# Optimization experiments

Measured on AMD Instinct MI355X. Metric: run time of the kernel, lower is better.

Reference implementation:

```python
import jax, jax.numpy as jnp
import numpy as np

N_NODES = 100000
N_EDGES = 3200000
F_IN, F_HID, F_OUT = 1433, 16, 7


def setup_inputs() -> dict:
    key = jax.random.key(0)
    k1, k2, k3, k4, k5, k6 = jax.random.split(key, 6)
    x = jax.random.normal(k1, (N_NODES, F_IN), dtype=jnp.float32)
    edge_index = jax.random.randint(k2, (2, N_EDGES), 0, N_NODES, dtype=jnp.int64)
    # Glorot-style init for GCNConv weights, zeros for bias (PyG default)
    W1 = jax.random.normal(k3, (F_IN, F_HID), dtype=jnp.float32) * (1.0 / np.sqrt(F_IN))
    b1 = jnp.zeros((F_HID,), dtype=jnp.float32)
    W2 = jax.random.normal(k4, (F_HID, F_OUT), dtype=jnp.float32) * (1.0 / np.sqrt(F_HID))
    b2 = jnp.zeros((F_OUT,), dtype=jnp.float32)
    return {"x": x, "edge_index": edge_index, "W1": W1, "b1": b1, "W2": W2, "b2": b2}


def _gcn_conv(x, W, b, src, dst, deg_inv_sqrt):
    # x: [N, Fin] -> [N, Fout]; src/dst: [E+N] (self-loops included)
    h = x @ W  # linear transform first (PyG GCNConv)
    norm = deg_inv_sqrt[src] * deg_inv_sqrt[dst]  # symmetric normalization
    msg = h[src] * norm[:, None]  # gather + scale
    agg = jax.ops.segment_sum(msg, dst, num_segments=x.shape[0])  # scatter-add at targets
    return agg + b


def reference(x, edge_index, W1, b1, W2, b2):
    n = x.shape[0]
    loops = jnp.arange(n, dtype=edge_index.dtype)
    src = jnp.concatenate([edge_index[0], loops])  # source nodes j
    dst = jnp.concatenate([edge_index[1], loops])  # target nodes i
    # degree over targets (with self-loops), unit edge weights
    deg = jax.ops.segment_sum(jnp.ones_like(src, dtype=x.dtype), dst, num_segments=n)
    deg_inv_sqrt = jnp.where(deg > 0, jax.lax.rsqrt(deg), 0.0)

    h = _gcn_conv(x, W1, b1, src, dst, deg_inv_sqrt)
    h = jax.nn.relu(h)
    # dropout is identity in eval mode
    h = _gcn_conv(h, W2, b2, src, dst, deg_inv_sqrt)
    return jax.nn.log_softmax(h, axis=1)
```

## Files before the change

### kernel.cpp

```cpp
#include <hip/hip_runtime.h>
#include <hip/hip_bf16.h>
#include <hip/hip_cooperative_groups.h>

namespace cg = cooperative_groups;

#define F_IN 1433
#define F_HID 16
#define F_OUT 7
#define KSTEPS 45

typedef __bf16 bf16x8 __attribute__((ext_vector_type(8)));
typedef float f32x4 __attribute__((ext_vector_type(4)));
typedef int i32x4 __attribute__((ext_vector_type(4)));
typedef unsigned short u16;
typedef unsigned int u32;

static __device__ __forceinline__ float bf2f(u16 b) {
    return __builtin_bit_cast(float, (u32)b << 16);
}
static __device__ __forceinline__ u16 f2bf(float f) {
    u32 u = __builtin_bit_cast(u32, f);
    u32 r = u + 0x7FFFu + ((u >> 16) & 1u);
    return (u16)(r >> 16);
}
static __device__ __forceinline__ int clampN(int v, int N) {
    return ((unsigned)v < (unsigned)N) ? v : 0;
}

static __device__ __forceinline__ void subset_bar(int* cnt, int target) {
    __syncthreads();
    if (threadIdx.x == 0) {
        __threadfence();
        __hip_atomic_fetch_add(cnt, 1, __ATOMIC_RELEASE, __HIP_MEMORY_SCOPE_AGENT);
        while (__hip_atomic_load(cnt, __ATOMIC_ACQUIRE, __HIP_MEMORY_SCOPE_AGENT) < target) {
            __builtin_amdgcn_s_sleep(8);
        }
        __threadfence();
    }
    __syncthreads();
}


static __device__ __forceinline__ void dev_stage_lw(const void* W1, int isbf, u16* lw, int tid) {
    const u16* W1u = (const u16*)W1;
    const float* W1f = (const float*)W1;
    for (int idx = tid; idx < KSTEPS * 512; idx += 256) {
        int j = idx & 7, lane = (idx >> 3) & 63, ks = idx >> 9;
        int quad = lane >> 4, n = lane & 15;
        int k = ks * 32 + quad * 8 + j;
        u16 w = 0;
        if (k < F_IN) w = isbf ? W1u[k * 16 + n] : f2bf(W1f[k * 16 + n]);
        lw[idx] = w;
    }
}

template <int ISBF>
static __device__ void dev_gemm(const u16* xu, const float* xf, const u16* lw,
                                float* __restrict__ hn, int N, int tid, int bid, int grid) {
    int wave = tid >> 6, lane = tid & 63;
    int quad = lane >> 4, m = lane & 15;
    int ntiles = (N + 63) / 64;
    int k0 = quad * 8;

    for (int tb = bid; tb < ntiles; tb += grid) {
        int base = tb * 64 + wave * 16;
        int row = base + m;
        int rowc = row < N ? row : N - 1;
        const u16* xru = xu + (size_t)rowc * F_IN;
        const float* xrf = xf + (size_t)rowc * F_IN;

        f32x4 acc = {0.f, 0.f, 0.f, 0.f};
        for (int ks = 0; ks < KSTEPS - 1; ks++) {
            u16 e[8];
            if (ISBF) {
                const u16* xp = xru + k0 + ks * 32;
#pragma unroll
                for (int j = 0; j < 8; j++) e[j] = xp[j];
            } else {
                const float* xp = xrf + k0 + ks * 32;
#pragma unroll
                for (int j = 0; j < 8; j++) e[j] = f2bf(xp[j]);
            }
            i32x4 wv = {(int)((u32)e[0] | ((u32)e[1] << 16)),
                        (int)((u32)e[2] | ((u32)e[3] << 16)),
                        (int)((u32)e[4] | ((u32)e[5] << 16)),
                        (int)((u32)e[6] | ((u32)e[7] << 16))};
            bf16x8 a = __builtin_bit_cast(bf16x8, wv);
            bf16x8 b = __builtin_bit_cast(bf16x8, *(const i32x4*)(&lw[ks * 512 + lane * 8]));
            acc = __builtin_amdgcn_mfma_f32_16x16x32_bf16(a, b, acc, 0, 0, 0);
        }
        {
            int ks = KSTEPS - 1;
            int kb = ks * 32 + k0;
            u16 e[8];
#pragma unroll
            for (int j = 0; j < 8; j++) {
                int k = kb + j;
                e[j] = (k < F_IN) ? (ISBF ? xru[k] : f2bf(xrf[k])) : (u16)0;
            }
            i32x4 wv = {(int)((u32)e[0] | ((u32)e[1] << 16)),
                        (int)((u32)e[2] | ((u32)e[3] << 16)),
                        (int)((u32)e[4] | ((u32)e[5] << 16)),
                        (int)((u32)e[6] | ((u32)e[7] << 16))};
            bf16x8 a = __builtin_bit_cast(bf16x8, wv);
            bf16x8 b = __builtin_bit_cast(bf16x8, *(const i32x4*)(&lw[ks * 512 + lane * 8]));
            acc = __builtin_amdgcn_mfma_f32_16x16x32_bf16(a, b, acc, 0, 0, 0);
        }
#pragma unroll
        for (int r = 0; r < 4; r++) {
            int orow = base + quad * 4 + r;
            if (orow < N) hn[(size_t)orow * 16 + m] = acc[r];
        }
    }
}

static __device__ void dev_agg1(const float* __restrict__ hn, const int* __restrict__ csr,
                                const int* __restrict__ rowoff, const int* __restrict__ deg,
                                const float* __restrict__ dis, const void* __restrict__ b1,
                                const void* __restrict__ W2, int isbf,
                                float* __restrict__ tn, int N, int bid, int grid, int tid) {
    int lane = tid & 63;
    int c = tid & 15, g = tid >> 4;
    float bc = isbf ? bf2f(((const u16*)b1)[c]) : ((const float*)b1)[c];
    float w2c[16];
#pragma unroll
    for (int k = 0; k < 16; k++) {
        float w = 0.f;
        if (c < 7) w = isbf ? bf2f(((const u16*)W2)[k * 7 + c]) : ((const float*)W2)[k * 7 + c];
        w2c[k] = w;
    }
    for (int v = bid * 16 + g; v < N; v += grid * 16) {
        float dv = dis[v];
        float acc = hn[(size_t)v * 16 + c] * dv;
        int s0 = rowoff[v], d = deg[v];
        const int* cp = csr + s0;
        float a1 = 0.f, a2 = 0.f, a3 = 0.f;
        int i = 0;
        for (; i + 4 <= d; i += 4) {
            int sA = clampN(cp[i], N), sB = clampN(cp[i + 1], N);
            int sC = clampN(cp[i + 2], N), sD = clampN(cp[i + 3], N);
            acc += hn[(size_t)sA * 16 + c] * dis[sA];
            a1 += hn[(size_t)sB * 16 + c] * dis[sB];
            a2 += hn[(size_t)sC * 16 + c] * dis[sC];
            a3 += hn[(size_t)sD * 16 + c] * dis[sD];
        }
        for (; i < d; i++) {
            int s = clampN(cp[i], N);
            acc += hn[(size_t)s * 16 + c] * dis[s];
        }
        acc += (a1 + a2) + a3;
        float y = fmaxf(acc * dv + bc, 0.f);
        float s = 0.f;
#pragma unroll
        for (int k = 0; k < 16; k++) s += __shfl(y, (lane & 48) + k, 64) * w2c[k];
        if (c < 8) tn[(size_t)v * 8 + c] = (c < 7) ? s * dv : 0.f;
    }
}

static __device__ void dev_agg2(const float* __restrict__ tn, const int* __restrict__ csr,
                                const int* __restrict__ rowoff, const int* __restrict__ deg,
                                const float* __restrict__ dis, const void* __restrict__ b2,
                                int isbf, void* __restrict__ out, int N, int bid, int grid,
                                int tid) {
    int c = tid & 7, g = tid >> 3;
    float bc = 0.f;
    if (c < 7) bc = isbf ? bf2f(((const u16*)b2)[c]) : ((const float*)b2)[c];
    for (int v = bid * 32 + g; v < N; v += grid * 32) {
        float acc = tn[(size_t)v * 8 + c];
        int s0 = rowoff[v], d = deg[v];
        const int* cp = csr + s0;
        float a1 = 0.f, a2 = 0.f, a3 = 0.f;
        int i = 0;
        for (; i + 4 <= d; i += 4) {
            int sA = clampN(cp[i], N), sB = clampN(cp[i + 1], N);
            int sC = clampN(cp[i + 2], N), sD = clampN(cp[i + 3], N);
            acc += tn[(size_t)sA * 8 + c];
            a1 += tn[(size_t)sB * 8 + c];
            a2 += tn[(size_t)sC * 8 + c];
            a3 += tn[(size_t)sD * 8 + c];
        }
        for (; i < d; i++) acc += tn[(size_t)clampN(cp[i], N) * 8 + c];
        acc += (a1 + a2) + a3;

        float z = (c < 7) ? (acc * dis[v] + bc) : -1e30f;
        float mx = z;
#pragma unroll
        for (int o = 1; o < 8; o <<= 1) mx = fmaxf(mx, __shfl_xor(mx, o, 8));
        float ex = (c < 7) ? expf(z - mx) : 0.f;
        float sm = ex;
#pragma unroll
        for (int o = 1; o < 8; o <<= 1) sm += __shfl_xor(sm, o, 8);
        sm = fmaxf(sm, 1e-30f);
        if (c < 7) {
            float res = z - mx - logf(sm);
            if (isbf)
                ((u16*)out)[(size_t)v * 7 + c] = f2bf(res);
            else
                ((float*)out)[(size_t)v * 7 + c] = res;
        }
    }
}


struct MegaArgs {
    const void* x;
    const int* ei;
    const void* W1;
    const void* b1;
    const void* W2;
    const void* b2;
    int* flags;
    int* cnt;
    int* deg;
    int* rowoff;
    int* fill;
    int* bsum;
    float* dis;
    int* csr;
    float* hn;
    float* tn;
    void* out;
    int N;
    int E;
};

__global__ __launch_bounds__(256) void k_mega(MegaArgs a) {
    cg::grid_group gg = cg::this_grid();
    int tid = threadIdx.x;
    int b = blockIdx.x;
    int G = gridDim.x;

    __shared__ int sflags[2];
    __shared__ __align__(16) u16 lw[KSTEPS * 512];
    __shared__ int sscan[256];
    __shared__ int swsum[4];

    for (int i = b * 256 + tid; i < a.N; i += G * 256) a.deg[i] = 0;
    if (b == 0) {
        if (tid == 0) a.cnt[0] = 0;
        if (tid < 64) {
            u16 v = ((const u16*)a.x)[tid];
            int e = (v >> 7) & 0xFF;
            unsigned long long mb = __ballot(e >= 100 && e <= 140);
            unsigned long long mz = __ballot(a.ei[2 * tid + 1] == 0);
            if (tid == 0) {
                a.flags[0] = (__popcll(mb) >= 56) ? 1 : 0;
                a.flags[1] = (__popcll(mz) >= 48) ? 1 : 0;
            }
        }
    }
    gg.sync();

    if (tid == 0) {
        sflags[0] = a.flags[0];
        sflags[1] = a.flags[1];
    }
    __syncthreads();
    int isbf = sflags[0], sh = sflags[1];

    int G2 = G >> 1;
    int nb = G - G2;
    if (b < G2) {
        dev_stage_lw(a.W1, isbf, lw, tid);
        __syncthreads();
        if (isbf)
            dev_gemm<1>((const u16*)a.x, (const float*)a.x, lw, a.hn, a.N, tid, b, G2);
        else
            dev_gemm<0>((const u16*)a.x, (const float*)a.x, lw, a.hn, a.N, tid, b, G2);
    } else {
        int lb = b - G2;
        for (int i = lb * 256 + tid; i < a.E; i += nb * 256) {
            int d = a.ei[(size_t)(a.E + i) << sh];
            atomicAdd(&a.deg[clampN(d, a.N)], 1);
        }
        subset_bar(a.cnt, nb * 1);
        int chunk = (a.N + nb - 1) / nb;
        int q = (chunk + 255) / 256;
        int base = lb * chunk;
        int nend = base + chunk;
        if (nend > a.N) nend = a.N;
        int tot = 0;
        for (int jj = 0; jj < q; jj++) {
            int node = base + tid * q + jj;
            if (node < nend) tot += a.deg[node];
        }
        sscan[tid] = tot;
        __syncthreads();
        for (int o = 1; o < 256; o <<= 1) {
            int xv = (tid >= o) ? sscan[tid - o] : 0;
            __syncthreads();
            sscan[tid] += xv;
            __syncthreads();
        }
        int incl = sscan[tid];
        if (tid == 255) a.bsum[lb] = incl;
        __syncthreads();
        sscan[tid] = incl - tot;
        subset_bar(a.cnt, nb * 2);
        int part = 0;
        for (int j = tid; j < lb; j += 256) part += a.bsum[j];
        for (int o = 32; o > 0; o >>= 1) part += __shfl_down(part, o, 64);
        if ((tid & 63) == 0) swsum[tid >> 6] = part;
        __syncthreads();
        int off = swsum[0] + swsum[1] + swsum[2] + swsum[3];
        int run = off + sscan[tid];
        for (int jj = 0; jj < q; jj++) {
            int node = base + tid * q + jj;
            if (node < nend) {
                int dn = a.deg[node];
                a.rowoff[node] = run;
                a.fill[node] = run;
                a.dis[node] = rsqrtf((float)(dn + 1));
                run += dn;
            }
        }
        subset_bar(a.cnt, nb * 3);
        for (int i = lb * 256 + tid; i < a.E; i += nb * 256) {
            int d = a.ei[(size_t)(a.E + i) << sh];
            int s = a.ei[(size_t)i << sh];
            int slot = atomicAdd(&a.fill[clampN(d, a.N)], 1);
            if (slot >= 0 && slot < a.E) a.csr[slot] = clampN(s, a.N);
        }
    }
    gg.sync();

    dev_agg1(a.hn, a.csr, a.rowoff, a.deg, a.dis, a.b1, a.W2, isbf, a.tn, a.N, b, G, tid);
    gg.sync();

    dev_agg2(a.tn, a.csr, a.rowoff, a.deg, a.dis, a.b2, isbf, a.out, a.N, b, G, tid);
}


__global__ __launch_bounds__(256) void k_init(const u16* __restrict__ xu,
                                              const int* __restrict__ ei,
                                              int* __restrict__ flags,
                                              int* __restrict__ deg, int N) {
    int i = blockIdx.x * 256 + threadIdx.x;
    if (i < N) deg[i] = 0;
    if (blockIdx.x == 0 && threadIdx.x < 64) {
        int t = threadIdx.x;
        u16 v = xu[t];
        int e = (v >> 7) & 0xFF;
        unsigned long long mb = __ballot(e >= 100 && e <= 140);
        unsigned long long mz = __ballot(ei[2 * t + 1] == 0);
        if (t == 0) {
            flags[0] = (__popcll(mb) >= 56) ? 1 : 0;
            flags[1] = (__popcll(mz) >= 48) ? 1 : 0;
        }
    }
}

__global__ __launch_bounds__(256) void k_deg(const int* __restrict__ ei,
                                             const int* __restrict__ flags,
                                             int* __restrict__ deg, int E, int N) {
    int sh = flags[1];
    int i = blockIdx.x * 256 + threadIdx.x;
    if (i < E) {
        int d = ei[(size_t)(E + i) << sh];
        atomicAdd(&deg[clampN(d, N)], 1);
    }
}

__global__ __launch_bounds__(256) void k_scan1(const int* __restrict__ deg,
                                               int* __restrict__ rowoff,
                                               int* __restrict__ bsum, int N) {
    __shared__ int s[256];
    int t = threadIdx.x, i = blockIdx.x * 256 + t;
    int v = (i < N) ? deg[i] : 0;
    s[t] = v;
    __syncthreads();
    for (int o = 1; o < 256; o <<= 1) {
        int x = 0;
        if (t >= o) x = s[t - o];
        __syncthreads();
        s[t] += x;
        __syncthreads();
    }
    if (i < N) rowoff[i] = s[t] - v;
    if (t == 255) bsum[blockIdx.x] = s[255];
}

__global__ __launch_bounds__(1024) void k_scan2(const int* __restrict__ bsum,
                                                int* __restrict__ bscan, int NB) {
    __shared__ int s[1024];
    int t = threadIdx.x;
    int v = (t < NB) ? bsum[t] : 0;
    s[t] = v;
    __syncthreads();
    for (int o = 1; o < 1024; o <<= 1) {
        int x = 0;
        if (t >= o) x = s[t - o];
        __syncthreads();
        s[t] += x;
        __syncthreads();
    }
    if (t < NB) bscan[t] = s[t] - v;
}

__global__ __launch_bounds__(256) void k_scan3(const int* __restrict__ deg,
                                               int* __restrict__ rowoff,
                                               const int* __restrict__ bscan,
                                               int* __restrict__ fill,
                                               float* __restrict__ dis, int N) {
    int i = blockIdx.x * 256 + threadIdx.x;
    if (i >= N) return;
    int ro = rowoff[i] + bscan[blockIdx.x];
    rowoff[i] = ro;
    fill[i] = ro;
    dis[i] = rsqrtf((float)(deg[i] + 1));
}

__global__ __launch_bounds__(256) void k_fill(const int* __restrict__ ei,
                                              const int* __restrict__ flags,
                                              int* __restrict__ fill,
                                              int* __restrict__ csr, int E, int N) {
    int sh = flags[1];
    int i = blockIdx.x * 256 + threadIdx.x;
    if (i < E) {
        int d = ei[(size_t)(E + i) << sh];
        int s = ei[(size_t)i << sh];
        int slot = atomicAdd(&fill[clampN(d, N)], 1);
        if (slot >= 0 && slot < E) csr[slot] = clampN(s, N);
    }
}

__global__ __launch_bounds__(256) void k_gemm1(const void* __restrict__ x,
                                               const void* __restrict__ W1,
                                               const int* __restrict__ flags,
                                               float* __restrict__ hn, int N) {
    __shared__ __align__(16) u16 lw[KSTEPS * 512];
    int tid = threadIdx.x;
    int isbf = flags[0];
    dev_stage_lw(W1, isbf, lw, tid);
    __syncthreads();
    if (isbf)
        dev_gemm<1>((const u16*)x, (const float*)x, lw, hn, N, tid, blockIdx.x, gridDim.x);
    else
        dev_gemm<0>((const u16*)x, (const float*)x, lw, hn, N, tid, blockIdx.x, gridDim.x);
}

__global__ __launch_bounds__(256) void k_agg1(const float* __restrict__ hn,
                                              const int* __restrict__ csr,
                                              const int* __restrict__ rowoff,
                                              const int* __restrict__ deg,
                                              const float* __restrict__ dis,
                                              const void* __restrict__ b1,
                                              const void* __restrict__ W2,
                                              const int* __restrict__ flags,
                                              float* __restrict__ tn, int N) {
    dev_agg1(hn, csr, rowoff, deg, dis, b1, W2, flags[0], tn, N, blockIdx.x, gridDim.x,
             threadIdx.x);
}

__global__ __launch_bounds__(256) void k_agg2(const float* __restrict__ tn,
                                              const int* __restrict__ csr,
                                              const int* __restrict__ rowoff,
                                              const int* __restrict__ deg,
                                              const float* __restrict__ dis,
                                              const void* __restrict__ b2,
                                              const int* __restrict__ flags,
                                              void* __restrict__ out, int N) {
    dev_agg2(tn, csr, rowoff, deg, dis, b2, flags[0], out, N, blockIdx.x, gridDim.x,
             threadIdx.x);
}


extern "C" void kernel_launch(void* const* d_in, const int* in_sizes, int n_in,
                              void* d_out, int out_size, void* d_ws, size_t ws_size,
                              hipStream_t stream) {
    const void* x = d_in[0];
    const int* ei = (const int*)d_in[1];
    const void* W1 = d_in[2];
    const void* b1 = d_in[3];
    const void* W2 = d_in[4];
    const void* b2 = d_in[5];

    int N = in_sizes[0] / F_IN;
    int E = in_sizes[1] / 2;

    char* p = (char*)d_ws;
    size_t off = 0;
    auto alloc = [&](size_t bytes) -> void* {
        off = (off + 255) & ~(size_t)255;
        void* r = p + off;
        off += bytes;
        return r;
    };
    int* flags = (int*)alloc(256);
    int* cnt = (int*)alloc(256);
    int* deg = (int*)alloc((size_t)N * 4);
    int* rowoff = (int*)alloc((size_t)N * 4);
    int* fill = (int*)alloc((size_t)N * 4);
    int* bsum = (int*)alloc(1024 * 4);
    int* bscan = (int*)alloc(1024 * 4);
    float* dis = (float*)alloc((size_t)N * 4);
    int* csr = (int*)alloc((size_t)E * 4);
    float* hn = (float*)alloc((size_t)N * 16 * 4);
    float* tn = (float*)alloc((size_t)N * 8 * 4);
    (void)ws_size;
    (void)n_in;
    (void)out_size;

    static int s_mb = -1;
    if (s_mb < 0) {
        int mb = 0;
        if (hipOccupancyMaxActiveBlocksPerMultiprocessor(
                &mb, reinterpret_cast<const void*>(&k_mega), 256, 0) != hipSuccess ||
            mb < 1)
            mb = 0;
        s_mb = mb;
    }
    int grid = s_mb * 256;
    if (grid > 1024) grid = 1024;

    bool ok = false;
    if (grid >= 8) {
        MegaArgs ha = {x,    ei,  W1,   b1,  W2, b2,  flags, cnt, deg,
                       rowoff, fill, bsum, dis, csr, hn, tn,  d_out, N,   E};
        void* params[] = {&ha};
        ok = (hipLaunchCooperativeKernel(reinterpret_cast<void*>(&k_mega), dim3(grid),
                                         dim3(256), params, 0, stream) == hipSuccess);
        if (!ok) (void)hipGetLastError();
    }

    if (!ok) {
        int gE = (E + 255) / 256;
        int gN = (N + 255) / 256;
        k_init<<<gN, 256, 0, stream>>>((const u16*)x, ei, flags, deg, N);
        k_deg<<<gE, 256, 0, stream>>>(ei, flags, deg, E, N);
        k_scan1<<<gN, 256, 0, stream>>>(deg, rowoff, bsum, N);
        k_scan2<<<1, 1024, 0, stream>>>(bsum, bscan, gN);
        k_scan3<<<gN, 256, 0, stream>>>(deg, rowoff, bscan, fill, dis, N);
        k_fill<<<gE, 256, 0, stream>>>(ei, flags, fill, csr, E, N);
        int ntiles = (N + 63) / 64;
        int gg = ntiles < 768 ? ntiles : 768;
        k_gemm1<<<gg, 256, 0, stream>>>(x, W1, flags, hn, N);
        k_agg1<<<(N + 15) / 16, 256, 0, stream>>>(hn, csr, rowoff, deg, dis, b1, W2, flags, tn, N);
        k_agg2<<<(N + 31) / 32, 256, 0, stream>>>(tn, csr, rowoff, deg, dis, b2, flags, d_out, N);
    }
}
```

Measured before the change: 1.329 ms.

## Serialize mega-kernel phases with atomic barriers and prescale GEMM output by degree

Replaces the cooperative-launch mega kernel, which overlapped the GEMM on half the grid with CSR construction on the other half, with a normally launched kernel. All blocks now run every phase in sequence, separated by custom atomic grid barriers, and flag detection moves into a tiny pre-kernel. The GEMM now multiplies its output rows by deg^-1/2, so the layer-1 aggregation no longer gathers dis per neighbor, and the A-fragment loads are vectorized and software-prefetched one step ahead. The grid size is now derived from the device's CU count. This relies on all blocks being co-resident without a cooperative launch, and the barriers bail out after a spin limit. It also gives up the GEMM/CSR overlap in exchange for using the full grid in each phase.

Result: slower. 1.732 ms (+30.3%).

```diff
diff --git a/kernel.cpp b/kernel.cpp
--- a/kernel.cpp
+++ b/kernel.cpp
@@ -1,8 +1,5 @@
 #include <hip/hip_runtime.h>
 #include <hip/hip_bf16.h>
-#include <hip/hip_cooperative_groups.h>
-
-namespace cg = cooperative_groups;
 
 #define F_IN 1433
 #define F_HID 16
@@ -27,13 +24,15 @@
     return ((unsigned)v < (unsigned)N) ? v : 0;
 }
 
-static __device__ __forceinline__ void subset_bar(int* cnt, int target) {
+static __device__ __forceinline__ void gbar(int* cnt, int target) {
     __syncthreads();
     if (threadIdx.x == 0) {
         __threadfence();
         __hip_atomic_fetch_add(cnt, 1, __ATOMIC_RELEASE, __HIP_MEMORY_SCOPE_AGENT);
+        unsigned spins = 0;
         while (__hip_atomic_load(cnt, __ATOMIC_ACQUIRE, __HIP_MEMORY_SCOPE_AGENT) < target) {
-            __builtin_amdgcn_s_sleep(8);
+            __builtin_amdgcn_s_sleep(2);
+            if (++spins > (1u << 24)) break;
         }
         __threadfence();
     }
@@ -55,8 +54,29 @@
 }
 
 template <int ISBF>
+static __device__ __forceinline__ i32x4 load_afrag(const u16* xru, const float* xrf, int kb) {
+    if (ISBF) {
+        i32x4 wv;
+        __builtin_memcpy(&wv, xru + kb, 16);
+        return wv;
+    } else {
+        float f[8];
+        __builtin_memcpy(f, xrf + kb, 32);
+        u16 e[8];
+#pragma unroll
+        for (int j = 0; j < 8; j++) e[j] = f2bf(f[j]);
+        i32x4 wv = {(int)((u32)e[0] | ((u32)e[1] << 16)),
+                    (int)((u32)e[2] | ((u32)e[3] << 16)),
+                    (int)((u32)e[4] | ((u32)e[5] << 16)),
+                    (int)((u32)e[6] | ((u32)e[7] << 16))};
+        return wv;
+    }
+}
+
+template <int ISBF>
 static __device__ void dev_gemm(const u16* xu, const float* xf, const u16* lw,
-                                float* __restrict__ hn, int N, int tid, int bid, int grid) {
+                                const float* __restrict__ dis, float* __restrict__ hn,
+                                int N, int tid, int bid, int grid) {
     int wave = tid >> 6, lane = tid & 63;
     int quad = lane >> 4, m = lane & 15;
     int ntiles = (N + 63) / 64;
@@ -70,22 +90,17 @@
         const float* xrf = xf + (size_t)rowc * F_IN;
 
         f32x4 acc = {0.f, 0.f, 0.f, 0.f};
-        for (int ks = 0; ks < KSTEPS - 1; ks++) {
-            u16 e[8];
-            if (ISBF) {
-                const u16* xp = xru + k0 + ks * 32;
-#pragma unroll
-                for (int j = 0; j < 8; j++) e[j] = xp[j];
-            } else {
-                const float* xp = xrf + k0 + ks * 32;
-#pragma unroll
-                for (int j = 0; j < 8; j++) e[j] = f2bf(xp[j]);
-            }
-            i32x4 wv = {(int)((u32)e[0] | ((u32)e[1] << 16)),
-                        (int)((u32)e[2] | ((u32)e[3] << 16)),
-                        (int)((u32)e[4] | ((u32)e[5] << 16)),
-                        (int)((u32)e[6] | ((u32)e[7] << 16))};
-            bf16x8 a = __builtin_bit_cast(bf16x8, wv);
+        i32x4 cur = load_afrag<ISBF>(xru, xrf, k0);
+        for (int ks = 0; ks < KSTEPS - 2; ks++) {
+            i32x4 nxt = load_afrag<ISBF>(xru, xrf, k0 + (ks + 1) * 32);
+            bf16x8 a = __builtin_bit_cast(bf16x8, cur);
+            bf16x8 b = __builtin_bit_cast(bf16x8, *(const i32x4*)(&lw[ks * 512 + lane * 8]));
+            acc = __builtin_amdgcn_mfma_f32_16x16x32_bf16(a, b, acc, 0, 0, 0);
+            cur = nxt;
+        }
+        {
+            int ks = KSTEPS - 2;
+            bf16x8 a = __builtin_bit_cast(bf16x8, cur);
             bf16x8 b = __builtin_bit_cast(bf16x8, *(const i32x4*)(&lw[ks * 512 + lane * 8]));
             acc = __builtin_amdgcn_mfma_f32_16x16x32_bf16(a, b, acc, 0, 0, 0);
         }
@@ -109,7 +124,7 @@
 #pragma unroll
         for (int r = 0; r < 4; r++) {
             int orow = base + quad * 4 + r;
-            if (orow < N) hn[(size_t)orow * 16 + m] = acc[r];
+            if (orow < N) hn[(size_t)orow * 16 + m] = acc[r] * dis[orow];
         }
     }
 }
@@ -130,8 +145,7 @@
         w2c[k] = w;
     }
     for (int v = bid * 16 + g; v < N; v += grid * 16) {
-        float dv = dis[v];
-        float acc = hn[(size_t)v * 16 + c] * dv;
+        float acc = hn[(size_t)v * 16 + c];
         int s0 = rowoff[v], d = deg[v];
         const int* cp = csr + s0;
         float a1 = 0.f, a2 = 0.f, a3 = 0.f;
@@ -139,16 +153,15 @@
         for (; i + 4 <= d; i += 4) {
             int sA = clampN(cp[i], N), sB = clampN(cp[i + 1], N);
             int sC = clampN(cp[i + 2], N), sD = clampN(cp[i + 3], N);
-            acc += hn[(size_t)sA * 16 + c] * dis[sA];
-            a1 += hn[(size_t)sB * 16 + c] * dis[sB];
-            a2 += hn[(size_t)sC * 16 + c] * dis[sC];
-            a3 += hn[(size_t)sD * 16 + c] * dis[sD];
-        }
-        for (; i < d; i++) {
-            int s = clampN(cp[i], N);
-            acc += hn[(size_t)s * 16 + c] * dis[s];
-        }
+            acc += hn[(size_t)sA * 16 + c];
+            a1 += hn[(size_t)sB * 16 + c];
+            a2 += hn[(size_t)sC * 16 + c];
+            a3 += hn[(size_t)sD * 16 + c];
+        }
+        for (; i < d; i++) acc += hn[(size_t)clampN(cp[i], N) * 16 + c];
         acc += (a1 + a2) + a3;
+
+        float dv = dis[v];
         float y = fmaxf(acc * dv + bc, 0.f);
         float s = 0.f;
 #pragma unroll
@@ -202,6 +215,23 @@
 }
 
 
+__global__ __launch_bounds__(64) void k_pre(const u16* __restrict__ xu,
+                                            const int* __restrict__ ei,
+                                            int* __restrict__ flags,
+                                            int* __restrict__ cnt) {
+    int t = threadIdx.x;
+    if (t == 0) cnt[0] = 0;
+    u16 v = xu[t];
+    int e = (v >> 7) & 0xFF;
+    unsigned long long mb = __ballot(e >= 100 && e <= 140);
+    unsigned long long mz = __ballot(ei[2 * t + 1] == 0);
+    if (t == 0) {
+        flags[0] = (__popcll(mb) >= 56) ? 1 : 0;
+        flags[1] = (__popcll(mz) >= 48) ? 1 : 0;
+    }
+}
+
+
 struct MegaArgs {
     const void* x;
     const int* ei;
@@ -224,8 +254,7 @@
     int E;
 };
 
-__global__ __launch_bounds__(256) void k_mega(MegaArgs a) {
-    cg::grid_group gg = cg::this_grid();
+__global__ __launch_bounds__(256) void k_mega2(MegaArgs a) {
     int tid = threadIdx.x;
     int b = blockIdx.x;
     int G = gridDim.x;
@@ -235,22 +264,6 @@
     __shared__ int sscan[256];
     __shared__ int swsum[4];
 
-    for (int i = b * 256 + tid; i < a.N; i += G * 256) a.deg[i] = 0;
-    if (b == 0) {
-        if (tid == 0) a.cnt[0] = 0;
-        if (tid < 64) {
-            u16 v = ((const u16*)a.x)[tid];
-            int e = (v >> 7) & 0xFF;
-            unsigned long long mb = __ballot(e >= 100 && e <= 140);
-            unsigned long long mz = __ballot(a.ei[2 * tid + 1] == 0);
-            if (tid == 0) {
-                a.flags[0] = (__popcll(mb) >= 56) ? 1 : 0;
-                a.flags[1] = (__popcll(mz) >= 48) ? 1 : 0;
-            }
-        }
-    }
-    gg.sync();
-
     if (tid == 0) {
         sflags[0] = a.flags[0];
         sflags[1] = a.flags[1];
@@ -258,27 +271,23 @@
     __syncthreads();
     int isbf = sflags[0], sh = sflags[1];
 
-    int G2 = G >> 1;
-    int nb = G - G2;
-    if (b < G2) {
-        dev_stage_lw(a.W1, isbf, lw, tid);
-        __syncthreads();
-        if (isbf)
-            dev_gemm<1>((const u16*)a.x, (const float*)a.x, lw, a.hn, a.N, tid, b, G2);
-        else
-            dev_gemm<0>((const u16*)a.x, (const float*)a.x, lw, a.hn, a.N, tid, b, G2);
-    } else {
-        int lb = b - G2;
-        for (int i = lb * 256 + tid; i < a.E; i += nb * 256) {
-            int d = a.ei[(size_t)(a.E + i) << sh];
-            atomicAdd(&a.deg[clampN(d, a.N)], 1);
-        }
-        subset_bar(a.cnt, nb * 1);
-        int chunk = (a.N + nb - 1) / nb;
-        int q = (chunk + 255) / 256;
-        int base = lb * chunk;
-        int nend = base + chunk;
-        if (nend > a.N) nend = a.N;
+    dev_stage_lw(a.W1, isbf, lw, tid);
+
+    for (int i = b * 256 + tid; i < a.N; i += G * 256) a.deg[i] = 0;
+    gbar(a.cnt, G * 1);
+
+    for (int i = b * 256 + tid; i < a.E; i += G * 256) {
+        int d = a.ei[(size_t)(a.E + i) << sh];
+        atomicAdd(&a.deg[clampN(d, a.N)], 1);
+    }
+    gbar(a.cnt, G * 2);
+
+    int chunk = (a.N + G - 1) / G;
+    int q = (chunk + 255) / 256;
+    int base = b * chunk;
+    int nend = base + chunk;
+    if (nend > a.N) nend = a.N;
+    {
         int tot = 0;
         for (int jj = 0; jj < q; jj++) {
             int node = base + tid * q + jj;
@@ -293,12 +302,15 @@
             __syncthreads();
         }
         int incl = sscan[tid];
-        if (tid == 255) a.bsum[lb] = incl;
+        if (tid == 255) a.bsum[b] = incl;
         __syncthreads();
         sscan[tid] = incl - tot;
-        subset_bar(a.cnt, nb * 2);
+    }
+    gbar(a.cnt, G * 3);
+
+    {
         int part = 0;
-        for (int j = tid; j < lb; j += 256) part += a.bsum[j];
+        for (int j = tid; j < b; j += 256) part += a.bsum[j];
         for (int o = 32; o > 0; o >>= 1) part += __shfl_down(part, o, 64);
         if ((tid & 63) == 0) swsum[tid >> 6] = part;
         __syncthreads();
@@ -314,18 +326,25 @@
                 run += dn;
             }
         }
-        subset_bar(a.cnt, nb * 3);
-        for (int i = lb * 256 + tid; i < a.E; i += nb * 256) {
-            int d = a.ei[(size_t)(a.E + i) << sh];
-            int s = a.ei[(size_t)i << sh];
-            int slot = atomicAdd(&a.fill[clampN(d, a.N)], 1);
-            if (slot >= 0 && slot < a.E) a.csr[slot] = clampN(s, a.N);
-        }
-    }
-    gg.sync();
+    }
+    gbar(a.cnt, G * 4);
+
+    for (int i = b * 256 + tid; i < a.E; i += G * 256) {
+        int d = a.ei[(size_t)(a.E + i) << sh];
+        int s = a.ei[(size_t)i << sh];
+        int slot = atomicAdd(&a.fill[clampN(d, a.N)], 1);
+        if (slot >= 0 && slot < a.E) a.csr[slot] = clampN(s, a.N);
+    }
+    gbar(a.cnt, G * 5);
+
+    if (isbf)
+        dev_gemm<1>((const u16*)a.x, (const float*)a.x, lw, a.dis, a.hn, a.N, tid, b, G);
+    else
+        dev_gemm<0>((const u16*)a.x, (const float*)a.x, lw, a.dis, a.hn, a.N, tid, b, G);
+    gbar(a.cnt, G * 6);
 
     dev_agg1(a.hn, a.csr, a.rowoff, a.deg, a.dis, a.b1, a.W2, isbf, a.tn, a.N, b, G, tid);
-    gg.sync();
+    gbar(a.cnt, G * 7);
 
     dev_agg2(a.tn, a.csr, a.rowoff, a.deg, a.dis, a.b2, isbf, a.out, a.N, b, G, tid);
 }
@@ -427,6 +446,7 @@
 __global__ __launch_bounds__(256) void k_gemm1(const void* __restrict__ x,
                                                const void* __restrict__ W1,
                                                const int* __restrict__ flags,
+                                               const float* __restrict__ dis,
                                                float* __restrict__ hn, int N) {
     __shared__ __align__(16) u16 lw[KSTEPS * 512];
     int tid = threadIdx.x;
@@ -434,9 +454,9 @@
     dev_stage_lw(W1, isbf, lw, tid);
     __syncthreads();
     if (isbf)
-        dev_gemm<1>((const u16*)x, (const float*)x, lw, hn, N, tid, blockIdx.x, gridDim.x);
+        dev_gemm<1>((const u16*)x, (const float*)x, lw, dis, hn, N, tid, blockIdx.x, gridDim.x);
     else
-        dev_gemm<0>((const u16*)x, (const float*)x, lw, hn, N, tid, blockIdx.x, gridDim.x);
+        dev_gemm<0>((const u16*)x, (const float*)x, lw, dis, hn, N, tid, blockIdx.x, gridDim.x);
 }
 
 __global__ __launch_bounds__(256) void k_agg1(const float* __restrict__ hn,
@@ -491,8 +511,8 @@
     int* deg = (int*)alloc((size_t)N * 4);
     int* rowoff = (int*)alloc((size_t)N * 4);
     int* fill = (int*)alloc((size_t)N * 4);
-    int* bsum = (int*)alloc(1024 * 4);
-    int* bscan = (int*)alloc(1024 * 4);
+    int* bsum = (int*)alloc(2048 * 4);
+    int* bscan = (int*)alloc(2048 * 4);
     float* dis = (float*)alloc((size_t)N * 4);
     int* csr = (int*)alloc((size_t)E * 4);
     float* hn = (float*)alloc((size_t)N * 16 * 4);
@@ -501,29 +521,27 @@
     (void)n_in;
     (void)out_size;
 
-    static int s_mb = -1;
-    if (s_mb < 0) {
-        int mb = 0;
+    static int s_grid = -1;
+    if (s_grid < 0) {
+        int mb = 0, cu = 256;
+        hipDeviceProp_t prop;
+        if (hipGetDeviceProperties(&prop, 0) == hipSuccess && prop.multiProcessorCount > 0)
+            cu = prop.multiProcessorCount;
         if (hipOccupancyMaxActiveBlocksPerMultiprocessor(
-                &mb, reinterpret_cast<const void*>(&k_mega), 256, 0) != hipSuccess ||
+                &mb, reinterpret_cast<const void*>(&k_mega2), 256, 0) != hipSuccess ||
             mb < 1)
             mb = 0;
-        s_mb = mb;
-    }
-    int grid = s_mb * 256;
-    if (grid > 1024) grid = 1024;
-
-    bool ok = false;
-    if (grid >= 8) {
-        MegaArgs ha = {x,    ei,  W1,   b1,  W2, b2,  flags, cnt, deg,
+        int g = mb * cu;
+        if (g > 1024) g = 1024;
+        s_grid = g;
+    }
+
+    if (s_grid >= 16) {
+        MegaArgs ha = {x,    ei,   W1,   b1,  W2,  b2, flags, cnt, deg,
                        rowoff, fill, bsum, dis, csr, hn, tn,  d_out, N,   E};
-        void* params[] = {&ha};
-        ok = (hipLaunchCooperativeKernel(reinterpret_cast<void*>(&k_mega), dim3(grid),
-                                         dim3(256), params, 0, stream) == hipSuccess);
-        if (!ok) (void)hipGetLastError();
-    }
-
-    if (!ok) {
+        k_pre<<<1, 64, 0, stream>>>((const u16*)x, ei, flags, cnt);
+        k_mega2<<<s_grid, 256, 0, stream>>>(ha);
+    } else {
         int gE = (E + 255) / 256;
         int gN = (N + 255) / 256;
         k_init<<<gN, 256, 0, stream>>>((const u16*)x, ei, flags, deg, N);
@@ -534,7 +552,7 @@
         k_fill<<<gE, 256, 0, stream>>>(ei, flags, fill, csr, E, N);
         int ntiles = (N + 63) / 64;
         int gg = ntiles < 768 ? ntiles : 768;
-        k_gemm1<<<gg, 256, 0, stream>>>(x, W1, flags, hn, N);
+        k_gemm1<<<gg, 256, 0, stream>>>(x, W1, flags, dis, hn, N);
         k_agg1<<<(N + 15) / 16, 256, 0, stream>>>(hn, csr, rowoff, deg, dis, b1, W2, flags, tn, N);
         k_agg2<<<(N + 31) / 32, 256, 0, stream>>>(tn, csr, rowoff, deg, dis, b2, flags, d_out, N);
     }
```
